# Optimization experiments

Hardware: AMD Instinct MI355X
Metric: run time of the kernel (lower is better)

The kernel has to match this reference:

```python
import jax, jax.numpy as jnp
import numpy as np

B, L, C, N = 8, 1024, 1024, 5000


def setup_inputs() -> dict:
    key = jax.random.key(0)
    k1, k2, k3 = jax.random.split(key, 3)
    z = jax.random.normal(k1, (B, L, C), dtype=jnp.float32)
    codebook = jax.random.normal(k2, (N, C), dtype=jnp.float32)
    mask = jax.random.bernoulli(k3, 0.9, (B, L))  # bool [B, L]
    return {"z": z, "mask": mask, "codebook": codebook}


def reference(z, mask, codebook):
    # pairwise squared L2 distance via the GEMM identity:
    # ||z - c||^2 = ||z||^2 + ||c||^2 - 2 z.c   (same math as broadcast-subtract-square-sum)
    z2 = jnp.sum(z * z, axis=-1, keepdims=True)        # [B, L, 1]
    c2 = jnp.sum(codebook * codebook, axis=-1)         # [N]
    cross = jnp.einsum('blc,nc->bln', z, codebook)     # [B, L, N]
    distance = z2 + c2 - 2.0 * cross                   # [B, L, N]
    indices = jnp.argmin(distance, axis=-1)            # [B, L] int
    quantized = codebook[indices]                      # gather -> [B, L, C]
    quantized = jnp.where(mask[..., None], quantized, 0.0)  # quantized[~mask] = 0
    commit_loss = jnp.float32(0.0)
    return quantized, indices, commit_loss
```

## Files before the change

kernel.cpp:

```cpp
#include <hip/hip_runtime.h>
#include <stdint.h>


#define M_TOTAL  8192
#define K_DIM    1024
#define N_REAL   5000
#define N_PAD    5120
#define NB_CNT   20
#define SLOTS    6
#define MARGIN   8.0f

typedef __attribute__((ext_vector_type(8))) short bf16x8;
typedef __attribute__((ext_vector_type(4))) float f32x4;
typedef unsigned long long u64;

__device__ __forceinline__ ushort f2bf(float x) {
  union { float f; uint32_t u; } v; v.f = x;
  uint32_t r = v.u + 0x7FFFu + ((v.u >> 16) & 1u);
  return (ushort)(r >> 16);
}

__device__ __forceinline__ void async16(void* lds, const void* g) {
  __builtin_amdgcn_global_load_lds(
      (const __attribute__((address_space(1))) void*)g,
      (__attribute__((address_space(3))) void*)lds, 16, 0, 0);
}

__device__ __forceinline__ uint32_t fenc(float f) {
  union { float f; uint32_t u; } v; v.f = f;
  return v.u ^ ((v.u >> 31) ? 0xFFFFFFFFu : 0x80000000u);
}
__device__ __forceinline__ float fdec(uint32_t e) {
  uint32_t u = e ^ ((e & 0x80000000u) ? 0x80000000u : 0xFFFFFFFFu);
  union { uint32_t u; float f; } v; v.u = u; return v.f;
}


__global__ __launch_bounds__(256) void convert_z(const float4* __restrict__ z4,
                                                 ushort* __restrict__ zb, int n4) {
  int i = blockIdx.x * blockDim.x + threadIdx.x;
  int stride = gridDim.x * blockDim.x;
  for (; i < n4; i += stride) {
    float4 v = z4[i];
    ushort4 u;
    u.x = f2bf(v.x); u.y = f2bf(v.y); u.z = f2bf(v.z); u.w = f2bf(v.w);
    *(ushort4*)&zb[(size_t)i * 4] = u;
  }
}

__global__ __launch_bounds__(256) void prep_cb(const float* __restrict__ cb,
                                               ushort* __restrict__ cbb,
                                               float* __restrict__ c2) {
  __shared__ float sred[4];
  const int row = blockIdx.x;
  const int tid = threadIdx.x;
  if (row >= N_REAL) {
    ushort4 zz; zz.x = zz.y = zz.z = zz.w = 0;
    *(ushort4*)&cbb[(size_t)row * K_DIM + tid * 4] = zz;
    if (tid == 0) c2[row] = 0.f;
    return;
  }
  float4 v = ((const float4*)(cb + (size_t)row * K_DIM))[tid];
  ushort4 u;
  u.x = f2bf(v.x); u.y = f2bf(v.y); u.z = f2bf(v.z); u.w = f2bf(v.w);
  *(ushort4*)&cbb[(size_t)row * K_DIM + tid * 4] = u;
  float s = v.x * v.x + v.y * v.y + v.z * v.z + v.w * v.w;
  #pragma unroll
  for (int off = 32; off; off >>= 1) s += __shfl_down(s, off);
  int wv = tid >> 6, ln = tid & 63;
  if (ln == 0) sred[wv] = s;
  __syncthreads();
  if (tid == 0) c2[row] = sred[0] + sred[1] + sred[2] + sred[3];
}


__global__ __launch_bounds__(512) void gemm_score(const ushort* __restrict__ A,
                                                  const ushort* __restrict__ Bm,
                                                  const float* __restrict__ c2,
                                                  u64* __restrict__ cand) {
  __shared__ __align__(16) char smem[131072];

  const int tid  = threadIdx.x;
  const int wave = tid >> 6, lane = tid & 63;
  const int wm = wave >> 2, wn = wave & 3;
  const int tM = blockIdx.y * 256;
  const int tN = blockIdx.x * 256;
  const int nb = blockIdx.x;

  f32x4 acc[8][4];
  #pragma unroll
  for (int i = 0; i < 8; ++i)
    #pragma unroll
    for (int j = 0; j < 4; ++j)
      acc[i][j] = (f32x4)0.f;

  const int o = tid * 16;

  auto stage = [&](int b, int k0) {
    char* dstA = smem + b * 65536;
    char* dstB = dstA + 32768;
    #pragma unroll
    for (int it = 0; it < 4; ++it) {
      int ob = o + it * 8192;
      int r  = ob >> 7;
      int cbyte = ob & 127;
      async16(dstA + ob, (const char*)A  + ((size_t)(tM + r) * K_DIM + k0) * 2 + cbyte);
      async16(dstB + ob, (const char*)Bm + ((size_t)(tN + r) * K_DIM + k0) * 2 + cbyte);
    }
  };

  auto compute = [&](int b) {
    const ushort* sA = (const ushort*)(smem + b * 65536);
    const ushort* sB = (const ushort*)(smem + b * 65536 + 32768);
    #pragma unroll
    for (int kk = 0; kk < 2; ++kk) {
      const int kcol = kk * 32 + (lane >> 4) * 8;
      bf16x8 af[8], bfr[4];
      #pragma unroll
      for (int f = 0; f < 8; ++f)
        af[f] = *(const bf16x8*)&sA[(wm * 128 + f * 16 + (lane & 15)) * 64 + kcol];
      #pragma unroll
      for (int f = 0; f < 4; ++f)
        bfr[f] = *(const bf16x8*)&sB[(wn * 64 + f * 16 + (lane & 15)) * 64 + kcol];
      #pragma unroll
      for (int i = 0; i < 8; ++i)
        #pragma unroll
        for (int j = 0; j < 4; ++j)
          acc[i][j] = __builtin_amdgcn_mfma_f32_16x16x32_bf16(af[i], bfr[j], acc[i][j], 0, 0, 0);
    }
  };

  stage(0, 0);
  __syncthreads();
  int cur = 0;
  for (int t = 0; t < (K_DIM / 64) - 1; ++t) {
    stage(cur ^ 1, (t + 1) * 64);
    compute(cur);
    __syncthreads();
    cur ^= 1;
  }
  compute(cur);

  __syncthreads();
  u64 (*scand)[SLOTS] = (u64 (*)[SLOTS])smem;
  int* scnt = (int*)(smem + 12288);
  if (tid < 256) {
    scnt[tid] = 0;
    #pragma unroll
    for (int s = 0; s < SLOTS; ++s) scand[tid][s] = ~0ull;
  }
  __syncthreads();

  const int cl = lane & 15, rg = lane >> 4;
  int   ncol[4];
  float c2v[4];
  #pragma unroll
  for (int j = 0; j < 4; ++j) {
    ncol[j] = tN + wn * 64 + j * 16 + cl;
    c2v[j]  = (ncol[j] < N_REAL) ? c2[ncol[j]] : 0.f;
  }

  #pragma unroll
  for (int i = 0; i < 8; ++i) {
    #pragma unroll
    for (int r = 0; r < 4; ++r) {
      float bv = 3.4e38f; int bc = 0x7fffffff;
      #pragma unroll
      for (int j = 0; j < 4; ++j) {
        float sc = (ncol[j] < N_REAL) ? (c2v[j] - 2.0f * acc[i][j][r]) : 3.4e38f;
        if (sc < bv || (sc == bv && ncol[j] < bc)) { bv = sc; bc = ncol[j]; }
      }
      #pragma unroll
      for (int off = 1; off < 16; off <<= 1) {
        float ov = __shfl_xor(bv, off);
        int   oc = __shfl_xor(bc, off);
        if (ov < bv || (ov == bv && oc < bc)) { bv = ov; bc = oc; }
      }
      if (cl == 0) {
        const int lr = wm * 128 + i * 16 + rg * 4 + r;
        u64 pk = ((u64)fenc(bv) << 32) | (uint32_t)bc;
        atomicMin(&scand[lr][0], pk);
      }
    }
  }
  __syncthreads();

  #pragma unroll
  for (int i = 0; i < 8; ++i) {
    #pragma unroll
    for (int r = 0; r < 4; ++r) {
      const int lr = wm * 128 + i * 16 + rg * 4 + r;
      const u64 mn = scand[lr][0];
      const float thr  = fdec((uint32_t)(mn >> 32)) + MARGIN;
      const int mincol = (int)(mn & 0xFFFFFFFFu);
      #pragma unroll
      for (int j = 0; j < 4; ++j) {
        if (ncol[j] < N_REAL) {
          float sc = c2v[j] - 2.0f * acc[i][j][r];
          if (sc <= thr && ncol[j] != mincol) {
            int p = atomicAdd(&scnt[lr], 1);
            if (p < SLOTS - 1)
              scand[lr][1 + p] = ((u64)fenc(sc) << 32) | (uint32_t)ncol[j];
          }
        }
      }
    }
  }
  __syncthreads();

  if (tid < 256) {
    const size_t base = ((size_t)(tM + tid) * NB_CNT + nb) * SLOTS;
    #pragma unroll
    for (int s = 0; s < SLOTS; ++s) cand[base + s] = scand[tid][s];
  }
}


__global__ __launch_bounds__(256) void finalize(const u64* __restrict__ cand,
                                                const float* __restrict__ z,
                                                const float* __restrict__ cb,
                                                const int* __restrict__ mask,
                                                float* __restrict__ out_q,
                                                float* __restrict__ out_i,
                                                float* __restrict__ out_loss) {
  __shared__ u64 swm[4];
  __shared__ float sthr;
  __shared__ int scols[64];
  __shared__ int scnt2;
  __shared__ double sdv[4];
  __shared__ double sbestd;
  __shared__ int    sbesti;

  const int tid = threadIdx.x;
  const int m   = blockIdx.x;
  const int wv = tid >> 6, ln = tid & 63;
  const u64* row = cand + (size_t)m * (NB_CNT * SLOTS);

  const u64 e = (tid < NB_CNT * SLOTS) ? row[tid] : ~0ull;

  u64 g = (tid < NB_CNT * SLOTS && (tid % SLOTS) == 0) ? e : ~0ull;
  #pragma unroll
  for (int off = 32; off; off >>= 1) {
    u64 o = __shfl_down(g, off);
    if (o < g) g = o;
  }
  if (ln == 0) swm[wv] = g;
  __syncthreads();
  if (tid == 0) {
    u64 gg = swm[0];
    for (int w = 1; w < 4; ++w) if (swm[w] < gg) gg = swm[w];
    sthr = fdec((uint32_t)(gg >> 32)) + MARGIN;
    scnt2 = 0;
  }
  __syncthreads();

  if (tid < NB_CNT * SLOTS) {
    float sc = fdec((uint32_t)(e >> 32));
    if (sc <= sthr) {
      int p = atomicAdd(&scnt2, 1);
      if (p < 64) scols[p] = (int)(e & 0xFFFFFFFFu);
    }
  }
  __syncthreads();
  int nc = scnt2 < 64 ? scnt2 : 64;

  if (tid == 0) { sbestd = 1e300; sbesti = 0x7fffffff; }
  __syncthreads();
  const float4 zv = ((const float4*)(z + (size_t)m * K_DIM))[tid];
  for (int c = 0; c < nc; ++c) {
    const int n = scols[c];
    float4 cv = ((const float4*)(cb + (size_t)n * K_DIM))[tid];
    double lsum = (double)cv.x * ((double)cv.x - 2.0 * (double)zv.x)
                + (double)cv.y * ((double)cv.y - 2.0 * (double)zv.y)
                + (double)cv.z * ((double)cv.z - 2.0 * (double)zv.z)
                + (double)cv.w * ((double)cv.w - 2.0 * (double)zv.w);
    #pragma unroll
    for (int off = 32; off; off >>= 1) lsum += __shfl_down(lsum, off);
    if (ln == 0) sdv[wv] = lsum;
    __syncthreads();
    if (tid == 0) {
      double s = sdv[0] + sdv[1] + sdv[2] + sdv[3];
      if (s < sbestd || (s == sbestd && n < sbesti)) { sbestd = s; sbesti = n; }
    }
    __syncthreads();
  }

  const int bidx = sbesti;
  if (tid == 0) out_i[m] = (float)bidx;
  const int mk = mask[m];
  float4 qz; qz.x = qz.y = qz.z = qz.w = 0.f;
  float4 src = ((const float4*)(cb + (size_t)bidx * K_DIM))[tid];
  ((float4*)(out_q + (size_t)m * K_DIM))[tid] = mk ? src : qz;
  if (m == 0 && tid == 0) *out_loss = 0.0f;
}


extern "C" void kernel_launch(void* const* d_in, const int* in_sizes, int n_in,
                              void* d_out, int out_size, void* d_ws, size_t ws_size,
                              hipStream_t stream) {
  const float* z    = (const float*)d_in[0];
  const int*   mask = (const int*)d_in[1];
  const float* cb   = (const float*)d_in[2];

  float* out      = (float*)d_out;
  float* out_q    = out;
  float* out_i    = out + (size_t)M_TOTAL * K_DIM;
  float* out_loss = out_i + M_TOTAL;

  char* ws = (char*)d_ws;
  ushort* zb   = (ushort*)(ws);
  ushort* cbb  = (ushort*)(ws + 16777216);
  float*  c2   = (float*)(ws + 27262976);
  u64*    cand = (u64*)(ws + 27283456);

  convert_z<<<2048, 256, 0, stream>>>((const float4*)z, zb, (M_TOTAL * K_DIM) / 4);
  prep_cb<<<N_PAD, 256, 0, stream>>>(cb, cbb, c2);

  dim3 g(N_PAD / 256, M_TOTAL / 256);
  gemm_score<<<g, 512, 0, stream>>>(zb, cbb, c2, cand);
  finalize<<<M_TOTAL, 256, 0, stream>>>(cand, z, cb, mask, out_q, out_i, out_loss);
}
```

Before: 297.4 us.

## Rewrite GEMM main loop with XOR-swizzled LDS, split-phase prefetch and priority hints

Restructures the bf16 MFMA main loop into four quarter phases, each interleaving async global-to-LDS loads of the next K-tile with MFMAs on the current tile. Partial vmcnt waits and raw barriers replace full syncthreads. LDS rows are XOR-swizzled to reduce bank conflicts on fragment reads, and s_setprio raises wave priority around MFMA bursts. The aim is to hide load latency and cut LDS conflicts. The cost is fragile manual waitcnt accounting and a launch_bounds hint of 2 blocks per CU, which may be unattainable with 128KB LDS and may push the compiler to spill registers.

Measured after the change: 281.3 us. 5.4% less time.

```diff
diff --git a/kernel.cpp b/kernel.cpp
--- a/kernel.cpp
+++ b/kernel.cpp
@@ -34,6 +34,8 @@
   uint32_t u = e ^ ((e & 0x80000000u) ? 0x80000000u : 0xFFFFFFFFu);
   union { uint32_t u; float f; } v; v.u = u; return v.f;
 }
+
+#define MFMA16(a, b, c) __builtin_amdgcn_mfma_f32_16x16x32_bf16((a), (b), (c), 0, 0, 0)
 
 
 __global__ __launch_bounds__(256) void convert_z(const float4* __restrict__ z4,
@@ -74,10 +76,10 @@
 }
 
 
-__global__ __launch_bounds__(512) void gemm_score(const ushort* __restrict__ A,
-                                                  const ushort* __restrict__ Bm,
-                                                  const float* __restrict__ c2,
-                                                  u64* __restrict__ cand) {
+__global__ __launch_bounds__(512, 2) void gemm_score(const ushort* __restrict__ A,
+                                                     const ushort* __restrict__ Bm,
+                                                     const float* __restrict__ c2,
+                                                     u64* __restrict__ cand) {
   __shared__ __align__(16) char smem[131072];
 
   const int tid  = threadIdx.x;
@@ -94,52 +96,140 @@
     for (int j = 0; j < 4; ++j)
       acc[i][j] = (f32x4)0.f;
 
-  const int o = tid * 16;
-
-  auto stage = [&](int b, int k0) {
-    char* dstA = smem + b * 65536;
-    char* dstB = dstA + 32768;
-    #pragma unroll
-    for (int it = 0; it < 4; ++it) {
-      int ob = o + it * 8192;
-      int r  = ob >> 7;
-      int cbyte = ob & 127;
-      async16(dstA + ob, (const char*)A  + ((size_t)(tM + r) * K_DIM + k0) * 2 + cbyte);
-      async16(dstB + ob, (const char*)Bm + ((size_t)(tN + r) * K_DIM + k0) * 2 + cbyte);
-    }
+  const int srow = tid >> 3;
+  const int scol = ((tid & 7) ^ (srow & 7)) * 8;
+  const int sdst = tid * 16;
+
+  const int lrow = lane & 15;
+  const int kgrp = (lane >> 4) * 16;
+  const int xorv = (lane & 7) << 4;
+
+  auto stA = [&](int b, int q, int k0) {
+    async16(smem + b * 65536 + q * 8192 + sdst,
+            (const char*)A + ((size_t)(tM + q * 64 + srow) * K_DIM + k0 + scol) * 2);
   };
-
-  auto compute = [&](int b) {
-    const ushort* sA = (const ushort*)(smem + b * 65536);
-    const ushort* sB = (const ushort*)(smem + b * 65536 + 32768);
-    #pragma unroll
-    for (int kk = 0; kk < 2; ++kk) {
-      const int kcol = kk * 32 + (lane >> 4) * 8;
-      bf16x8 af[8], bfr[4];
-      #pragma unroll
-      for (int f = 0; f < 8; ++f)
-        af[f] = *(const bf16x8*)&sA[(wm * 128 + f * 16 + (lane & 15)) * 64 + kcol];
-      #pragma unroll
-      for (int f = 0; f < 4; ++f)
-        bfr[f] = *(const bf16x8*)&sB[(wn * 64 + f * 16 + (lane & 15)) * 64 + kcol];
-      #pragma unroll
-      for (int i = 0; i < 8; ++i)
-        #pragma unroll
-        for (int j = 0; j < 4; ++j)
-          acc[i][j] = __builtin_amdgcn_mfma_f32_16x16x32_bf16(af[i], bfr[j], acc[i][j], 0, 0, 0);
-    }
+  auto stB = [&](int b, int q, int k0) {
+    async16(smem + b * 65536 + 32768 + q * 8192 + sdst,
+            (const char*)Bm + ((size_t)(tN + q * 64 + srow) * K_DIM + k0 + scol) * 2);
   };
-
-  stage(0, 0);
-  __syncthreads();
-  int cur = 0;
+  auto ldA = [&](int b, int i, int kk) {
+    return *(const bf16x8*)(smem + b * 65536 +
+           (wm * 128 + i * 16 + lrow) * 128 + ((kk * 64 + kgrp) ^ xorv));
+  };
+  auto ldB = [&](int b, int j, int kk) {
+    return *(const bf16x8*)(smem + b * 65536 + 32768 +
+           (wn * 64 + j * 16 + lrow) * 128 + ((kk * 64 + kgrp) ^ xorv));
+  };
+
+  bf16x8 aLo[4][2], aHi[4][2], bLo[2][2], bHi[2][2];
+
+  stB(0,0,0); stB(0,1,0); stB(0,2,0); stB(0,3,0);
+  stA(0,0,0); stA(0,2,0); stA(0,1,0); stA(0,3,0);
+
   for (int t = 0; t < (K_DIM / 64) - 1; ++t) {
-    stage(cur ^ 1, (t + 1) * 64);
-    compute(cur);
-    __syncthreads();
-    cur ^= 1;
-  }
-  compute(cur);
+    const int b = t & 1, nbf = b ^ 1;
+    const int k1 = (t + 1) * 64;
+
+    stB(nbf, 0, k1); stB(nbf, 1, k1);
+    asm volatile("s_waitcnt vmcnt(4)" ::: "memory");
+    __builtin_amdgcn_s_barrier();
+    #pragma unroll
+    for (int i = 0; i < 4; ++i) { aLo[i][0] = ldA(b,i,0); aLo[i][1] = ldA(b,i,1); }
+    #pragma unroll
+    for (int j = 0; j < 2; ++j) { bLo[j][0] = ldB(b,j,0); bLo[j][1] = ldB(b,j,1); }
+    __builtin_amdgcn_s_setprio(1);
+    #pragma unroll
+    for (int i = 0; i < 4; ++i)
+      #pragma unroll
+      for (int j = 0; j < 2; ++j) {
+        acc[i][j] = MFMA16(aLo[i][0], bLo[j][0], acc[i][j]);
+        acc[i][j] = MFMA16(aLo[i][1], bLo[j][1], acc[i][j]);
+      }
+    __builtin_amdgcn_s_setprio(0);
+
+    stB(nbf, 2, k1); stB(nbf, 3, k1);
+    #pragma unroll
+    for (int j = 0; j < 2; ++j) { bHi[j][0] = ldB(b,j+2,0); bHi[j][1] = ldB(b,j+2,1); }
+    __builtin_amdgcn_s_setprio(1);
+    #pragma unroll
+    for (int i = 0; i < 4; ++i)
+      #pragma unroll
+      for (int j = 0; j < 2; ++j) {
+        acc[i][j+2] = MFMA16(aLo[i][0], bHi[j][0], acc[i][j+2]);
+        acc[i][j+2] = MFMA16(aLo[i][1], bHi[j][1], acc[i][j+2]);
+      }
+    __builtin_amdgcn_s_setprio(0);
+
+    stA(nbf, 0, k1); stA(nbf, 2, k1);
+    asm volatile("s_waitcnt vmcnt(6)" ::: "memory");
+    __builtin_amdgcn_s_barrier();
+    #pragma unroll
+    for (int i = 0; i < 4; ++i) { aHi[i][0] = ldA(b,i+4,0); aHi[i][1] = ldA(b,i+4,1); }
+    #pragma unroll
+    for (int j = 0; j < 2; ++j) { bLo[j][0] = ldB(b,j,0); bLo[j][1] = ldB(b,j,1); }
+    __builtin_amdgcn_s_setprio(1);
+    #pragma unroll
+    for (int i = 0; i < 4; ++i)
+      #pragma unroll
+      for (int j = 0; j < 2; ++j) {
+        acc[i+4][j] = MFMA16(aHi[i][0], bLo[j][0], acc[i+4][j]);
+        acc[i+4][j] = MFMA16(aHi[i][1], bLo[j][1], acc[i+4][j]);
+      }
+    __builtin_amdgcn_s_setprio(0);
+
+    stA(nbf, 1, k1); stA(nbf, 3, k1);
+    #pragma unroll
+    for (int j = 0; j < 2; ++j) { bHi[j][0] = ldB(b,j+2,0); bHi[j][1] = ldB(b,j+2,1); }
+    __builtin_amdgcn_s_setprio(1);
+    #pragma unroll
+    for (int i = 0; i < 4; ++i)
+      #pragma unroll
+      for (int j = 0; j < 2; ++j) {
+        acc[i+4][j+2] = MFMA16(aHi[i][0], bHi[j][0], acc[i+4][j+2]);
+        acc[i+4][j+2] = MFMA16(aHi[i][1], bHi[j][1], acc[i+4][j+2]);
+      }
+    __builtin_amdgcn_s_setprio(0);
+    __builtin_amdgcn_s_barrier();
+  }
+
+  {
+    const int b = 1;
+    asm volatile("s_waitcnt vmcnt(2)" ::: "memory");
+    __builtin_amdgcn_s_barrier();
+    #pragma unroll
+    for (int i = 0; i < 4; ++i) { aLo[i][0] = ldA(b,i,0); aLo[i][1] = ldA(b,i,1); }
+    #pragma unroll
+    for (int j = 0; j < 2; ++j) { bLo[j][0] = ldB(b,j,0); bLo[j][1] = ldB(b,j,1); }
+    #pragma unroll
+    for (int i = 0; i < 4; ++i)
+      #pragma unroll
+      for (int j = 0; j < 2; ++j) {
+        acc[i][j] = MFMA16(aLo[i][0], bLo[j][0], acc[i][j]);
+        acc[i][j] = MFMA16(aLo[i][1], bLo[j][1], acc[i][j]);
+      }
+    #pragma unroll
+    for (int j = 0; j < 2; ++j) { bHi[j][0] = ldB(b,j+2,0); bHi[j][1] = ldB(b,j+2,1); }
+    #pragma unroll
+    for (int i = 0; i < 4; ++i)
+      #pragma unroll
+      for (int j = 0; j < 2; ++j) {
+        acc[i][j+2] = MFMA16(aLo[i][0], bHi[j][0], acc[i][j+2]);
+        acc[i][j+2] = MFMA16(aLo[i][1], bHi[j][1], acc[i][j+2]);
+      }
+    asm volatile("s_waitcnt vmcnt(0)" ::: "memory");
+    __builtin_amdgcn_s_barrier();
+    #pragma unroll
+    for (int i = 0; i < 4; ++i) { aHi[i][0] = ldA(b,i+4,0); aHi[i][1] = ldA(b,i+4,1); }
+    #pragma unroll
+    for (int i = 0; i < 4; ++i)
+      #pragma unroll
+      for (int j = 0; j < 2; ++j) {
+        acc[i+4][j] = MFMA16(aHi[i][0], bLo[j][0], acc[i+4][j]);
+        acc[i+4][j] = MFMA16(aHi[i][1], bLo[j][1], acc[i+4][j]);
+        acc[i+4][j+2] = MFMA16(aHi[i][0], bHi[j][0], acc[i+4][j+2]);
+        acc[i+4][j+2] = MFMA16(aHi[i][1], bHi[j][1], acc[i+4][j+2]);
+      }
+  }
 
   __syncthreads();
   u64 (*scand)[SLOTS] = (u64 (*)[SLOTS])smem;
```

## Restructure GEMM main loop into fine-grained ping-pong schedule with swizzled LDS

Applied to the files above, without the earlier changes.

Replaces the simple double-buffered stage/compute loop with a hand-scheduled pipeline. Each 64-wide K slice is split into A and B halves, and quarter-tile MFMA groups are interleaved with partial async global-to-LDS loads, explicit barriers, waitcnts and s_setprio. The LDS tile layout gains an XOR swizzle to cut bank conflicts on the fragment reads. Launch bounds are raised to request two blocks per CU, which caps registers per thread and could force spills of the large accumulator array.

After: 283.9 us. 4.5% less time.

```diff
diff --git a/kernel.cpp b/kernel.cpp
--- a/kernel.cpp
+++ b/kernel.cpp
@@ -34,6 +34,8 @@
   uint32_t u = e ^ ((e & 0x80000000u) ? 0x80000000u : 0xFFFFFFFFu);
   union { uint32_t u; float f; } v; v.u = u; return v.f;
 }
+
+#define MFMA16(a, b, c) __builtin_amdgcn_mfma_f32_16x16x32_bf16((a), (b), (c), 0, 0, 0)
 
 
 __global__ __launch_bounds__(256) void convert_z(const float4* __restrict__ z4,
@@ -74,10 +76,10 @@
 }
 
 
-__global__ __launch_bounds__(512) void gemm_score(const ushort* __restrict__ A,
-                                                  const ushort* __restrict__ Bm,
-                                                  const float* __restrict__ c2,
-                                                  u64* __restrict__ cand) {
+__global__ __launch_bounds__(512, 2) void gemm_score(const ushort* __restrict__ A,
+                                                     const ushort* __restrict__ Bm,
+                                                     const float* __restrict__ c2,
+                                                     u64* __restrict__ cand) {
   __shared__ __align__(16) char smem[131072];
 
   const int tid  = threadIdx.x;
@@ -94,52 +96,123 @@
     for (int j = 0; j < 4; ++j)
       acc[i][j] = (f32x4)0.f;
 
-  const int o = tid * 16;
-
-  auto stage = [&](int b, int k0) {
-    char* dstA = smem + b * 65536;
-    char* dstB = dstA + 32768;
-    #pragma unroll
-    for (int it = 0; it < 4; ++it) {
-      int ob = o + it * 8192;
-      int r  = ob >> 7;
-      int cbyte = ob & 127;
-      async16(dstA + ob, (const char*)A  + ((size_t)(tM + r) * K_DIM + k0) * 2 + cbyte);
-      async16(dstB + ob, (const char*)Bm + ((size_t)(tN + r) * K_DIM + k0) * 2 + cbyte);
-    }
-  };
-
-  auto compute = [&](int b) {
-    const ushort* sA = (const ushort*)(smem + b * 65536);
-    const ushort* sB = (const ushort*)(smem + b * 65536 + 32768);
-    #pragma unroll
-    for (int kk = 0; kk < 2; ++kk) {
-      const int kcol = kk * 32 + (lane >> 4) * 8;
-      bf16x8 af[8], bfr[4];
-      #pragma unroll
-      for (int f = 0; f < 8; ++f)
-        af[f] = *(const bf16x8*)&sA[(wm * 128 + f * 16 + (lane & 15)) * 64 + kcol];
-      #pragma unroll
-      for (int f = 0; f < 4; ++f)
-        bfr[f] = *(const bf16x8*)&sB[(wn * 64 + f * 16 + (lane & 15)) * 64 + kcol];
-      #pragma unroll
-      for (int i = 0; i < 8; ++i)
-        #pragma unroll
-        for (int j = 0; j < 4; ++j)
-          acc[i][j] = __builtin_amdgcn_mfma_f32_16x16x32_bf16(af[i], bfr[j], acc[i][j], 0, 0, 0);
-    }
-  };
-
-  stage(0, 0);
-  __syncthreads();
-  int cur = 0;
-  for (int t = 0; t < (K_DIM / 64) - 1; ++t) {
-    stage(cur ^ 1, (t + 1) * 64);
-    compute(cur);
-    __syncthreads();
-    cur ^= 1;
-  }
-  compute(cur);
+  const int sr   = tid >> 3;
+  const int sc   = ((tid & 7) ^ (sr & 7)) * 8;
+  const int sdst = tid * 16;
+  const int pn   = tid >> 8;
+  const int blr  = sr & 31;
+
+  auto stA = [&](int d, int h, int k0) {
+    char* dst = smem + d * 65536 + h * 16384;
+    async16(dst + sdst,
+            (const char*)A + ((size_t)(tM + h * 64 + sr) * K_DIM + k0 + sc) * 2);
+    async16(dst + 8192 + sdst,
+            (const char*)A + ((size_t)(tM + 128 + h * 64 + sr) * K_DIM + k0 + sc) * 2);
+  };
+  auto stB = [&](int d, int h, int k0) {
+    char* dst = smem + d * 65536 + 32768 + h * 16384;
+    async16(dst + sdst,
+            (const char*)Bm + ((size_t)(tN + pn * 64 + h * 32 + blr) * K_DIM + k0 + sc) * 2);
+    async16(dst + 8192 + sdst,
+            (const char*)Bm + ((size_t)(tN + (pn + 2) * 64 + h * 32 + blr) * K_DIM + k0 + sc) * 2);
+  };
+
+  const int lrow = lane & 15;
+  const int kgb  = (lane >> 4) * 16;
+  const int xorv = (lane & 7) << 4;
+  auto ldA8 = [&](int d, int h, int i, int kk) {
+    return *(const bf16x8*)(smem + d * 65536 + h * 16384 + wm * 8192
+                            + (i * 16 + lrow) * 128 + ((kk * 64 + kgb) ^ xorv));
+  };
+  auto ldB8 = [&](int d, int h, int jj, int kk) {
+    return *(const bf16x8*)(smem + d * 65536 + 32768 + h * 16384 + wn * 4096
+                            + (jj * 16 + lrow) * 128 + ((kk * 64 + kgb) ^ xorv));
+  };
+
+  bf16x8 ar[4][2], brL[2][2], brH[2][2];
+  auto rdA = [&](int d, int h) {
+    #pragma unroll
+    for (int i = 0; i < 4; ++i) { ar[i][0] = ldA8(d, h, i, 0); ar[i][1] = ldA8(d, h, i, 1); }
+  };
+  auto rdBL = [&](int d) {
+    #pragma unroll
+    for (int j = 0; j < 2; ++j) { brL[j][0] = ldB8(d, 0, j, 0); brL[j][1] = ldB8(d, 0, j, 1); }
+  };
+  auto rdBH = [&](int d) {
+    #pragma unroll
+    for (int j = 0; j < 2; ++j) { brH[j][0] = ldB8(d, 1, j, 0); brH[j][1] = ldB8(d, 1, j, 1); }
+  };
+  auto MMqL = [&](int hA) {
+    #pragma unroll
+    for (int i = 0; i < 4; ++i)
+      #pragma unroll
+      for (int j = 0; j < 2; ++j) {
+        acc[hA*4+i][j] = MFMA16(ar[i][0], brL[j][0], acc[hA*4+i][j]);
+        acc[hA*4+i][j] = MFMA16(ar[i][1], brL[j][1], acc[hA*4+i][j]);
+      }
+  };
+  auto MMqH = [&](int hA) {
+    #pragma unroll
+    for (int i = 0; i < 4; ++i)
+      #pragma unroll
+      for (int j = 0; j < 2; ++j) {
+        acc[hA*4+i][2+j] = MFMA16(ar[i][0], brH[j][0], acc[hA*4+i][2+j]);
+        acc[hA*4+i][2+j] = MFMA16(ar[i][1], brH[j][1], acc[hA*4+i][2+j]);
+      }
+  };
+
+#define BAR()    __builtin_amdgcn_s_barrier()
+#define LGKM0()  asm volatile("s_waitcnt lgkmcnt(0)" ::: "memory")
+#define PRIO1()  __builtin_amdgcn_s_setprio(1)
+#define PRIO0()  __builtin_amdgcn_s_setprio(0)
+
+  stA(0,0,0);  stB(0,1,0);  stB(0,0,0);  stA(0,1,0);
+  stA(1,0,64); stB(1,1,64); stB(1,0,64); stA(1,1,64);
+  asm volatile("s_waitcnt vmcnt(8)" ::: "memory");
+  BAR();
+
+  #pragma unroll 1
+  for (int it = 0; it < 7; ++it) {
+    const int kA = (2*it + 2) * 64;
+    const int kB = (2*it + 3) * 64;
+    rdA(0,0); rdBL(0);
+    BAR(); LGKM0(); PRIO1(); MMqL(0); PRIO0(); BAR();
+    rdBH(0); stA(0,0,kA);
+    BAR(); LGKM0(); PRIO1(); MMqH(0); PRIO0(); BAR();
+    rdA(0,1); rdBL(0); stB(0,1,kA);
+    BAR(); LGKM0(); PRIO1(); MMqL(1); PRIO0(); BAR();
+    stB(0,0,kA);
+    BAR(); LGKM0(); PRIO1(); MMqH(1); PRIO0();
+    asm volatile("s_waitcnt vmcnt(6)" ::: "memory");
+    BAR();
+    rdA(1,0); rdBL(1); stA(0,1,kA);
+    BAR(); LGKM0(); PRIO1(); MMqL(0); PRIO0(); BAR();
+    rdBH(1); stA(1,0,kB);
+    BAR(); LGKM0(); PRIO1(); MMqH(0); PRIO0(); BAR();
+    rdA(1,1); rdBL(1); stB(1,1,kB);
+    BAR(); LGKM0(); PRIO1(); MMqL(1); PRIO0(); BAR();
+    stB(1,0,kB); stA(1,1,kB);
+    BAR(); LGKM0(); PRIO1(); MMqH(1); PRIO0();
+    asm volatile("s_waitcnt vmcnt(8)" ::: "memory");
+    BAR();
+  }
+
+  rdA(0,0); rdBL(0);
+  BAR(); LGKM0(); PRIO1(); MMqL(0); PRIO0(); BAR();
+  rdBH(0);
+  BAR(); LGKM0(); PRIO1(); MMqH(0); PRIO0(); BAR();
+  rdA(0,1); rdBL(0);
+  BAR(); LGKM0(); PRIO1(); MMqL(1); PRIO0(); BAR();
+  BAR(); LGKM0(); PRIO1(); MMqH(1); PRIO0();
+  asm volatile("s_waitcnt vmcnt(0)" ::: "memory");
+  BAR();
+  rdA(1,0); rdBL(1);
+  BAR(); LGKM0(); PRIO1(); MMqL(0); PRIO0(); BAR();
+  rdBH(1);
+  BAR(); LGKM0(); PRIO1(); MMqH(0); PRIO0(); BAR();
+  rdA(1,1); rdBL(1);
+  BAR(); LGKM0(); PRIO1(); MMqL(1); PRIO0(); BAR();
+  PRIO1(); MMqH(1); PRIO0();
 
   __syncthreads();
   u64 (*scand)[SLOTS] = (u64 (*)[SLOTS])smem;
@@ -167,8 +240,8 @@
       float bv = 3.4e38f; int bc = 0x7fffffff;
       #pragma unroll
       for (int j = 0; j < 4; ++j) {
-        float sc = (ncol[j] < N_REAL) ? (c2v[j] - 2.0f * acc[i][j][r]) : 3.4e38f;
-        if (sc < bv || (sc == bv && ncol[j] < bc)) { bv = sc; bc = ncol[j]; }
+        float sc2 = (ncol[j] < N_REAL) ? (c2v[j] - 2.0f * acc[i][j][r]) : 3.4e38f;
+        if (sc2 < bv || (sc2 == bv && ncol[j] < bc)) { bv = sc2; bc = ncol[j]; }
       }
       #pragma unroll
       for (int off = 1; off < 16; off <<= 1) {
@@ -196,11 +269,11 @@
       #pragma unroll
       for (int j = 0; j < 4; ++j) {
         if (ncol[j] < N_REAL) {
-          float sc = c2v[j] - 2.0f * acc[i][j][r];
-          if (sc <= thr && ncol[j] != mincol) {
+          float sc2 = c2v[j] - 2.0f * acc[i][j][r];
+          if (sc2 <= thr && ncol[j] != mincol) {
             int p = atomicAdd(&scnt[lr], 1);
             if (p < SLOTS - 1)
-              scand[lr][1 + p] = ((u64)fenc(sc) << 32) | (uint32_t)ncol[j];
+              scand[lr][1 + p] = ((u64)fenc(sc2) << 32) | (uint32_t)ncol[j];
           }
         }
       }
```
